# Kernel optimization log

Measured on AMD Instinct MI355X. Metric: run time of the kernel, lower is better.

The kernel has to match this reference:

```python
import jax, jax.numpy as jnp
import numpy as np

B, C, T, H, HI = 256, 64, 512, 8, 3


def setup_inputs() -> dict:
    key = jax.random.key(0)
    ks = jax.random.split(key, 20)
    s = 0.1
    return {
        "x": jax.random.normal(ks[0], (B, C, T), jnp.float32),
        "m": jax.random.uniform(ks[1], (B, C, T), jnp.float32),
        "d": jax.random.uniform(ks[2], (B, C, T), jnp.float32),
        # interpolater params (per-channel blocks of the block-diagonal matrices)
        "Wf": jax.random.normal(ks[3], (C, H, H), jnp.float32) * s,
        "Vf": jax.random.normal(ks[4], (C, H, 3), jnp.float32) * s,
        "cf": jax.random.normal(ks[5], (C, H), jnp.float32) * s,
        "Wb": jax.random.normal(ks[6], (C, H, H), jnp.float32) * s,
        "Vb": jax.random.normal(ks[7], (C, H, 3), jnp.float32) * s,
        "cb": jax.random.normal(ks[8], (C, H), jnp.float32) * s,
        "U": jax.random.normal(ks[9], (C, 2 * H), jnp.float32) * s,
        "c0": jax.random.normal(ks[10], (C,), jnp.float32) * s,
        # imputer params (nn.Linear: y = x @ W.T + b)
        "V1_w": jax.random.normal(ks[11], (HI, C), jnp.float32) * s,
        "V2_w": jax.random.normal(ks[12], (HI, C), jnp.float32) * s,
        "U_w": jax.random.normal(ks[13], (HI, C), jnp.float32) * s,
        "U_b": jax.random.normal(ks[14], (HI,), jnp.float32) * s,
        "W_w": jax.random.normal(ks[15], (C, HI), jnp.float32) * s,
        "W_b": jax.random.normal(ks[16], (C,), jnp.float32) * s,
    }


def _mrnn_forward(x, m, d, Wf, Vf, cf, Wb, Vb, cb, U, c0,
                  V1_w, V2_w, U_w, U_b, W_w, W_b):
    act = jax.nn.relu
    Bv, Cv, Tv = x.shape
    Hv = Wf.shape[-1]
    # replication pad along time: [B,C,T] -> [B,C,T+2]
    pad = lambda a: jnp.pad(a, ((0, 0), (0, 0), (1, 1)), mode='edge')
    s = jnp.stack([pad(x), pad(m), pad(d)], axis=-1)        # [B,C,T+2,3]
    # forward scan consumes padded times 0..T-1; backward consumes T+1 down to 2
    in_f = jnp.moveaxis(s[:, :, :Tv], 2, 0)                 # [T,B,C,3]
    in_b = jnp.moveaxis(s[:, :, 2:Tv + 2][:, :, ::-1], 2, 0)  # [T,B,C,3]

    def make_step(W, V, c):
        def step(h, inp):  # h:[B,C,H] inp:[B,C,3]
            hn = act(jnp.einsum('chk,bck->bch', W, h)
                     + jnp.einsum('chj,bcj->bch', V, inp) + c)
            return hn, hn
        return step

    h0 = jnp.zeros((Bv, Cv, Hv), x.dtype)
    _, hf = jax.lax.scan(make_step(Wf, Vf, cf), h0, in_f)   # [T,B,C,H]
    _, hb = jax.lax.scan(make_step(Wb, Vb, cb), h0, in_b)
    hb = hb[::-1]  # align backward hiddens with time index

    x_est = act(jnp.einsum('ch,tbch->bct', U[:, :Hv], hf)
                + jnp.einsum('ch,tbch->bct', U[:, Hv:], hb)
                + c0[None, :, None])                        # [B,C,T]

    # imputer (time as batch dim); U weight has zeroed diagonal
    idx = jnp.arange(min(U_w.shape[0], Cv))
    Uz = U_w.at[idx, idx].set(0.0)
    h = act(jnp.swapaxes(x_est, 1, 2) @ V1_w.T
            + jnp.swapaxes(m, 1, 2) @ V2_w.T
            + jnp.swapaxes(x, 1, 2) @ Uz.T + U_b)           # [B,T,HI]
    out = h @ W_w.T + W_b                                   # [B,T,C]
    return jnp.swapaxes(out, 1, 2)                          # [B,C,T]


def reference(x, m, d, Wf, Vf, cf, Wb, Vb, cb, U, c0,
              V1_w, V2_w, U_w, U_b, W_w, W_b):
    return _mrnn_forward(x, m, d, Wf, Vf, cf, Wb, Vb, cb, U, c0,
                         V1_w, V2_w, U_w, U_b, W_w, W_b)
```

## Files before the change

### kernel.cpp

```cpp
#include <hip/hip_runtime.h>

constexpr int Tn = 512;
constexpr int Cn = 64;
constexpr int NS = 16384;

typedef float f2 __attribute__((ext_vector_type(2)));

template<int CTRL>
__device__ __forceinline__ float dppf(float v) {
    int i = __builtin_bit_cast(int, v);
    i = __builtin_amdgcn_mov_dpp(i, CTRL, 0xF, 0xF, true);
    return __builtin_bit_cast(float, i);
}
__device__ __forceinline__ f2 rot1(f2 v) {
    f2 r; r.x = dppf<0x39>(v.x); r.y = dppf<0x39>(v.y); return r;
}

#define QSTEP(xv, mv, dv, SGN) do {                                   \
    f2 hr = h;                                                        \
    f2 a0 = cbp + Vp0 * (xv);                                         \
    f2 a1 = Vp1 * (mv);                                               \
    a0 += Vp2 * (dv);                                                 \
    a0 += WA0 * hr.x;  a1 += WB0 * hr.y;                              \
    hr = rot1(hr);                                                    \
    a0 += WA1 * hr.x;  a1 += WB1 * hr.y;                              \
    hr = rot1(hr);                                                    \
    a0 += WA2 * hr.x;  a1 += WB2 * hr.y;                              \
    hr = rot1(hr);                                                    \
    a0 += WA3 * hr.x;  a1 += WB3 * hr.y;                              \
    f2 hn = a0 + a1;                                                  \
    hn.x = fmaxf(hn.x, 0.f); hn.y = fmaxf(hn.y, 0.f);                 \
    h = hn;                                                           \
    float pdv = Up.x * hn.x + Up.y * hn.y;                            \
    pdv += dppf<0xB1>(pdv);                                           \
    pdv += dppf<0x4E>(pdv);                                           \
    *op = pdv;                                                        \
    op SGN NS;                                                        \
} while (0)

#define GRP_F(X4, M4, D4) do {                                        \
    QSTEP(cx, cm, cd, +=);                                            \
    QSTEP((X4).x, (M4).x, (D4).x, +=);                                \
    QSTEP((X4).y, (M4).y, (D4).y, +=);                                \
    QSTEP((X4).z, (M4).z, (D4).z, +=);                                \
    cx = (X4).w; cm = (M4).w; cd = (D4).w;                            \
} while (0)

#define GRP_B(X4, M4, D4) do {                                        \
    QSTEP(cx, cm, cd, -=);                                            \
    QSTEP((X4).w, (M4).w, (D4).w, -=);                                \
    QSTEP((X4).z, (M4).z, (D4).z, -=);                                \
    QSTEP((X4).y, (M4).y, (D4).y, -=);                                \
    cx = (X4).x; cm = (M4).x; cd = (D4).x;                            \
} while (0)

__global__ __launch_bounds__(256, 2) void mrnn_scan(
    const float* __restrict__ x, const float* __restrict__ m, const float* __restrict__ d,
    const float* __restrict__ Wf, const float* __restrict__ Vf, const float* __restrict__ cf,
    const float* __restrict__ Wb, const float* __restrict__ Vb, const float* __restrict__ cbk,
    const float* __restrict__ U, float* __restrict__ accF, float* __restrict__ accB)
{
    const int g   = blockIdx.x * blockDim.x + threadIdx.x;
    const int q   = g & 3;
    const int sd  = g >> 2;
    const int dir = sd >> 14;
    const int seq = sd & 16383;
    const int c   = seq & 63;
    const long base = (long)seq * Tn;

    const float* W  = dir ? Wb  : Wf;
    const float* V  = dir ? Vb  : Vf;
    const float* cc = dir ? cbk : cf;

    const int r0 = 2*q, r1 = 2*q + 1;

    f2 WA0, WA1, WA2, WA3, WB0, WB1, WB2, WB3, Vp0, Vp1, Vp2, cbp, Up;
    {
        const float* Wc = W + c*64;
        int col;
        col = 2*((q+0)&3);
        WA0 = f2{Wc[r0*8+col],   Wc[r1*8+col]};
        WB0 = f2{Wc[r0*8+col+1], Wc[r1*8+col+1]};
        col = 2*((q+1)&3);
        WA1 = f2{Wc[r0*8+col],   Wc[r1*8+col]};
        WB1 = f2{Wc[r0*8+col+1], Wc[r1*8+col+1]};
        col = 2*((q+2)&3);
        WA2 = f2{Wc[r0*8+col],   Wc[r1*8+col]};
        WB2 = f2{Wc[r0*8+col+1], Wc[r1*8+col+1]};
        col = 2*((q+3)&3);
        WA3 = f2{Wc[r0*8+col],   Wc[r1*8+col]};
        WB3 = f2{Wc[r0*8+col+1], Wc[r1*8+col+1]};
    }
    Vp0 = f2{V[c*24 + r0*3 + 0], V[c*24 + r1*3 + 0]};
    Vp1 = f2{V[c*24 + r0*3 + 1], V[c*24 + r1*3 + 1]};
    Vp2 = f2{V[c*24 + r0*3 + 2], V[c*24 + r1*3 + 2]};
    cbp = f2{cc[c*8 + r0], cc[c*8 + r1]};
    Up  = f2{U[c*16 + dir*8 + r0], U[c*16 + dir*8 + r1]};

    f2 h = {0.f, 0.f};
    float cx, cm, cd;
    const float4* x4 = (const float4*)(x + base);
    const float4* m4 = (const float4*)(m + base);
    const float4* d4 = (const float4*)(d + base);
    float* op = (dir ? accB : accF) + seq;

    if (dir == 0) {
        float4 Ax = x4[0], Am = m4[0], Ad = d4[0];
        float4 Bx = x4[1], Bm = m4[1], Bd = d4[1];
        cx = Ax.x; cm = Am.x; cd = Ad.x;
        #pragma unroll 1
        for (int i = 0; i < 63; ++i) {
            float4 Txq = x4[2*i+2], Tmq = m4[2*i+2], Tdq = d4[2*i+2];
            GRP_F(Ax, Am, Ad);
            float4 Uxq = x4[2*i+3], Umq = m4[2*i+3], Udq = d4[2*i+3];
            GRP_F(Bx, Bm, Bd);
            Ax = Txq; Am = Tmq; Ad = Tdq;
            Bx = Uxq; Bm = Umq; Bd = Udq;
        }
        GRP_F(Ax, Am, Ad);
        GRP_F(Bx, Bm, Bd);
    } else {
        op += 511 * NS;
        float4 Ax = x4[127], Am = m4[127], Ad = d4[127];
        float4 Bx = x4[126], Bm = m4[126], Bd = d4[126];
        cx = Ax.w; cm = Am.w; cd = Ad.w;
        #pragma unroll 1
        for (int i = 0; i < 63; ++i) {
            float4 Txq = x4[125-2*i], Tmq = m4[125-2*i], Tdq = d4[125-2*i];
            GRP_B(Ax, Am, Ad);
            float4 Uxq = x4[124-2*i], Umq = m4[124-2*i], Udq = d4[124-2*i];
            GRP_B(Bx, Bm, Bd);
            Ax = Txq; Am = Tmq; Ad = Tdq;
            Bx = Uxq; Bm = Umq; Bd = Udq;
        }
        GRP_B(Ax, Am, Ad);
        GRP_B(Bx, Bm, Bd);
    }
}

__global__ __launch_bounds__(256, 2) void mrnn_mix(
    const float* __restrict__ x, const float* __restrict__ m,
    const float* __restrict__ accF, const float* __restrict__ accB,
    const float* __restrict__ c0, const float* __restrict__ V1w,
    const float* __restrict__ V2w, const float* __restrict__ Uw,
    const float* __restrict__ Ub, const float* __restrict__ Ww,
    const float* __restrict__ Wbias, float* __restrict__ out)
{
    const int bt = blockIdx.x * 256 + threadIdx.x;
    const int b = bt >> 9;
    const int t = bt & 511;

    const float4* aF4 = (const float4*)(accF + (size_t)t * NS + b * Cn);
    const float4* aB4 = (const float4*)(accB + (size_t)t * NS + b * Cn);
    const size_t xb = (size_t)b * (Cn * Tn) + t;

    float h0 = Ub[0], h1 = Ub[1], h2 = Ub[2];
    #pragma unroll
    for (int c4 = 0; c4 < 16; ++c4) {
        const float4 fa = aF4[c4];
        const float4 fb = aB4[c4];
        const float fav[4] = {fa.x, fa.y, fa.z, fa.w};
        const float fbv[4] = {fb.x, fb.y, fb.z, fb.w};
        #pragma unroll
        for (int j = 0; j < 4; ++j) {
            const int cch = 4*c4 + j;
            const float xe = fmaxf(fav[j] + fbv[j] + c0[cch], 0.f);
            const float mv = m[xb + (size_t)cch * Tn];
            const float xv = x[xb + (size_t)cch * Tn];
            const float u0 = (cch == 0) ? 0.f : Uw[0*Cn + cch];
            const float u1 = (cch == 1) ? 0.f : Uw[1*Cn + cch];
            const float u2 = (cch == 2) ? 0.f : Uw[2*Cn + cch];
            h0 += V1w[0*Cn + cch]*xe + V2w[0*Cn + cch]*mv + u0*xv;
            h1 += V1w[1*Cn + cch]*xe + V2w[1*Cn + cch]*mv + u1*xv;
            h2 += V1w[2*Cn + cch]*xe + V2w[2*Cn + cch]*mv + u2*xv;
        }
    }
    h0 = fmaxf(h0, 0.f); h1 = fmaxf(h1, 0.f); h2 = fmaxf(h2, 0.f);

    float* opt = out + (size_t)b * (Cn * Tn) + t;
    #pragma unroll
    for (int cch = 0; cch < Cn; ++cch) {
        opt[(size_t)cch * Tn] = Wbias[cch] + Ww[cch*3 + 0]*h0 + Ww[cch*3 + 1]*h1 + Ww[cch*3 + 2]*h2;
    }
}

extern "C" void kernel_launch(void* const* d_in, const int* in_sizes, int n_in,
                              void* d_out, int out_size, void* d_ws, size_t ws_size,
                              hipStream_t stream)
{
    const float* x   = (const float*)d_in[0];
    const float* m   = (const float*)d_in[1];
    const float* d   = (const float*)d_in[2];
    const float* Wf  = (const float*)d_in[3];
    const float* Vf  = (const float*)d_in[4];
    const float* cf  = (const float*)d_in[5];
    const float* Wb  = (const float*)d_in[6];
    const float* Vb  = (const float*)d_in[7];
    const float* cb  = (const float*)d_in[8];
    const float* U   = (const float*)d_in[9];
    const float* c0  = (const float*)d_in[10];
    const float* V1w = (const float*)d_in[11];
    const float* V2w = (const float*)d_in[12];
    const float* Uw  = (const float*)d_in[13];
    const float* Ub  = (const float*)d_in[14];
    const float* Ww  = (const float*)d_in[15];
    const float* Wb_ = (const float*)d_in[16];
    float* out = (float*)d_out;

    float* accF = (float*)d_ws;
    float* accB = accF + (size_t)Tn * NS;

    mrnn_scan<<<512, 256, 0, stream>>>(x, m, d, Wf, Vf, cf, Wb, Vb, cb, U, accF, accB);
    mrnn_mix<<<512, 256, 0, stream>>>(x, m, accF, accB, c0, V1w, V2w, Uw, Ub, Ww, Wb_, out);
}
```

Measured before the change: 116.8 us.

## Split recurrent scan to one hidden unit per lane using ds_swizzle broadcasts

The scan kernel now assigns 8 lanes per sequence, one hidden unit each, instead of 4 lanes holding two units. Each step broadcasts the 8 hidden values within the lane group with ds_swizzle and reduces the output projection through a 3-level swizzle tree, replacing the DPP rotations. The grid doubles and launch bounds target 4 blocks per CU to raise parallelism and occupancy on the serial time recurrence. ds_swizzle goes through the LDS crossbar and has higher latency than DPP, and every lane in a group of 8 now loads the same x/m/d stream and writes the same output, duplicating memory traffic.

```diff
diff --git a/kernel.cpp b/kernel.cpp
--- a/kernel.cpp
+++ b/kernel.cpp
@@ -4,67 +4,65 @@
 constexpr int Cn = 64;
 constexpr int NS = 16384;
 
-typedef float f2 __attribute__((ext_vector_type(2)));
-
-template<int CTRL>
-__device__ __forceinline__ float dppf(float v) {
+template<int OFF>
+__device__ __forceinline__ float swzf(float v) {
     int i = __builtin_bit_cast(int, v);
-    i = __builtin_amdgcn_mov_dpp(i, CTRL, 0xF, 0xF, true);
+    i = __builtin_amdgcn_ds_swizzle(i, OFF);
     return __builtin_bit_cast(float, i);
 }
-__device__ __forceinline__ f2 rot1(f2 v) {
-    f2 r; r.x = dppf<0x39>(v.x); r.y = dppf<0x39>(v.y); return r;
-}
 
-#define QSTEP(xv, mv, dv, SGN) do {                                   \
-    f2 hr = h;                                                        \
-    f2 a0 = cbp + Vp0 * (xv);                                         \
-    f2 a1 = Vp1 * (mv);                                               \
-    a0 += Vp2 * (dv);                                                 \
-    a0 += WA0 * hr.x;  a1 += WB0 * hr.y;                              \
-    hr = rot1(hr);                                                    \
-    a0 += WA1 * hr.x;  a1 += WB1 * hr.y;                              \
-    hr = rot1(hr);                                                    \
-    a0 += WA2 * hr.x;  a1 += WB2 * hr.y;                              \
-    hr = rot1(hr);                                                    \
-    a0 += WA3 * hr.x;  a1 += WB3 * hr.y;                              \
-    f2 hn = a0 + a1;                                                  \
-    hn.x = fmaxf(hn.x, 0.f); hn.y = fmaxf(hn.y, 0.f);                 \
-    h = hn;                                                           \
-    float pdv = Up.x * hn.x + Up.y * hn.y;                            \
-    pdv += dppf<0xB1>(pdv);                                           \
-    pdv += dppf<0x4E>(pdv);                                           \
-    *op = pdv;                                                        \
+#define OSTEP(xv, mv, dv, SGN) do {                                   \
+    float t0 = swzf<0x18>(h);                                         \
+    float t1 = swzf<0x38>(h);                                         \
+    float t2 = swzf<0x58>(h);                                         \
+    float t3 = swzf<0x78>(h);                                         \
+    float a = fmaf(Vr0, (xv), cb);                                    \
+    float b = Vr1 * (mv);                                             \
+    float e = Vr2 * (dv);                                             \
+    a = fmaf(W0, t0, a);  b = fmaf(W1, t1, b);  e = fmaf(W2, t2, e);  \
+    t0 = swzf<0x98>(h);                                               \
+    t1 = swzf<0xB8>(h);                                               \
+    t2 = swzf<0xD8>(h);                                               \
+    float t7 = swzf<0xF8>(h);                                         \
+    a = fmaf(W3, t3, a);                                              \
+    b = fmaf(W4, t0, b);  e = fmaf(W5, t1, e);                        \
+    a = fmaf(W6, t2, a);  b = fmaf(W7, t7, b);                        \
+    h = fmaxf(a + (b + e), 0.f);                                      \
+    float p = Ur * h;                                                 \
+    p += swzf<0x041F>(p);                                             \
+    p += swzf<0x081F>(p);                                             \
+    p += swzf<0x101F>(p);                                             \
+    *op = p;                                                          \
     op SGN NS;                                                        \
 } while (0)
 
 #define GRP_F(X4, M4, D4) do {                                        \
-    QSTEP(cx, cm, cd, +=);                                            \
-    QSTEP((X4).x, (M4).x, (D4).x, +=);                                \
-    QSTEP((X4).y, (M4).y, (D4).y, +=);                                \
-    QSTEP((X4).z, (M4).z, (D4).z, +=);                                \
+    OSTEP(cx, cm, cd, +=);                                            \
+    OSTEP((X4).x, (M4).x, (D4).x, +=);                                \
+    OSTEP((X4).y, (M4).y, (D4).y, +=);                                \
+    OSTEP((X4).z, (M4).z, (D4).z, +=);                                \
     cx = (X4).w; cm = (M4).w; cd = (D4).w;                            \
 } while (0)
 
 #define GRP_B(X4, M4, D4) do {                                        \
-    QSTEP(cx, cm, cd, -=);                                            \
-    QSTEP((X4).w, (M4).w, (D4).w, -=);                                \
-    QSTEP((X4).z, (M4).z, (D4).z, -=);                                \
-    QSTEP((X4).y, (M4).y, (D4).y, -=);                                \
+    OSTEP(cx, cm, cd, -=);                                            \
+    OSTEP((X4).w, (M4).w, (D4).w, -=);                                \
+    OSTEP((X4).z, (M4).z, (D4).z, -=);                                \
+    OSTEP((X4).y, (M4).y, (D4).y, -=);                                \
     cx = (X4).x; cm = (M4).x; cd = (D4).x;                            \
 } while (0)
 
-__global__ __launch_bounds__(256, 2) void mrnn_scan(
+__global__ __launch_bounds__(256, 4) void mrnn_scan(
     const float* __restrict__ x, const float* __restrict__ m, const float* __restrict__ d,
     const float* __restrict__ Wf, const float* __restrict__ Vf, const float* __restrict__ cf,
     const float* __restrict__ Wb, const float* __restrict__ Vb, const float* __restrict__ cbk,
     const float* __restrict__ U, float* __restrict__ accF, float* __restrict__ accB)
 {
     const int g   = blockIdx.x * blockDim.x + threadIdx.x;
-    const int q   = g & 3;
-    const int sd  = g >> 2;
-    const int dir = sd >> 14;
-    const int seq = sd & 16383;
+    const int r   = g & 7;
+    const int td  = g >> 3;
+    const int dir = td >> 14;
+    const int seq = td & 16383;
     const int c   = seq & 63;
     const long base = (long)seq * Tn;
 
@@ -72,32 +70,16 @@
     const float* V  = dir ? Vb  : Vf;
     const float* cc = dir ? cbk : cf;
 
-    const int r0 = 2*q, r1 = 2*q + 1;
+    const float* Wr = W + c*64 + r*8;
+    const float W0 = Wr[0], W1 = Wr[1], W2 = Wr[2], W3 = Wr[3];
+    const float W4 = Wr[4], W5 = Wr[5], W6 = Wr[6], W7 = Wr[7];
+    const float Vr0 = V[c*24 + r*3 + 0];
+    const float Vr1 = V[c*24 + r*3 + 1];
+    const float Vr2 = V[c*24 + r*3 + 2];
+    const float cb  = cc[c*8 + r];
+    const float Ur  = U[c*16 + dir*8 + r];
 
-    f2 WA0, WA1, WA2, WA3, WB0, WB1, WB2, WB3, Vp0, Vp1, Vp2, cbp, Up;
-    {
-        const float* Wc = W + c*64;
-        int col;
-        col = 2*((q+0)&3);
-        WA0 = f2{Wc[r0*8+col],   Wc[r1*8+col]};
-        WB0 = f2{Wc[r0*8+col+1], Wc[r1*8+col+1]};
-        col = 2*((q+1)&3);
-        WA1 = f2{Wc[r0*8+col],   Wc[r1*8+col]};
-        WB1 = f2{Wc[r0*8+col+1], Wc[r1*8+col+1]};
-        col = 2*((q+2)&3);
-        WA2 = f2{Wc[r0*8+col],   Wc[r1*8+col]};
-        WB2 = f2{Wc[r0*8+col+1], Wc[r1*8+col+1]};
-        col = 2*((q+3)&3);
-        WA3 = f2{Wc[r0*8+col],   Wc[r1*8+col]};
-        WB3 = f2{Wc[r0*8+col+1], Wc[r1*8+col+1]};
-    }
-    Vp0 = f2{V[c*24 + r0*3 + 0], V[c*24 + r1*3 + 0]};
-    Vp1 = f2{V[c*24 + r0*3 + 1], V[c*24 + r1*3 + 1]};
-    Vp2 = f2{V[c*24 + r0*3 + 2], V[c*24 + r1*3 + 2]};
-    cbp = f2{cc[c*8 + r0], cc[c*8 + r1]};
-    Up  = f2{U[c*16 + dir*8 + r0], U[c*16 + dir*8 + r1]};
-
-    f2 h = {0.f, 0.f};
+    float h = 0.f;
     float cx, cm, cd;
     const float4* x4 = (const float4*)(x + base);
     const float4* m4 = (const float4*)(m + base);
@@ -210,6 +192,6 @@
     float* accF = (float*)d_ws;
     float* accB = accF + (size_t)Tn * NS;
 
-    mrnn_scan<<<512, 256, 0, stream>>>(x, m, d, Wf, Vf, cf, Wb, Vb, cb, U, accF, accB);
+    mrnn_scan<<<1024, 256, 0, stream>>>(x, m, d, Wf, Vf, cf, Wb, Vb, cb, U, accF, accB);
     mrnn_mix<<<512, 256, 0, stream>>>(x, m, accF, accB, c0, V1w, V2w, Uw, Ub, Ww, Wb_, out);
 }
```

New measurement: 164.0 us. 1.4x slower.
